# Kernel tuning notes

Hardware: AMD Instinct MI355X
Metric: run time of the kernel (lower is better)

Reference implementation:

```python
import jax, jax.numpy as jnp
import numpy as np

N_NODES = 100000

def graph_conv(x, edge_index, w_root, w_rel, b):
    # PyG GraphConv (aggr='add'): out = aggr(x_j) @ W_rel + b + x @ W_root
    src, dst = edge_index[0], edge_index[1]
    msgs = x[src]                                   # [E, F_in] gather
    agg = jax.ops.segment_sum(msgs, dst, num_segments=N_NODES)  # [N, F_in] scatter-add
    return agg @ w_rel + b + x @ w_root             # [N, F_out]


def setup_inputs() -> dict:
    key = jax.random.key(0)
    ks = jax.random.split(key, 12)
    E = 1600000
    return {
        "x": jax.random.normal(ks[0], (N_NODES, 16), dtype=jnp.float32),
        "edge_index": jax.random.randint(ks[1], (2, E), 0, N_NODES, dtype=jnp.int64),
        "w_root1": jax.random.normal(ks[2], (16, 32), dtype=jnp.float32) * 0.1,
        "w_rel1": jax.random.normal(ks[3], (16, 32), dtype=jnp.float32) * 0.1,
        "b1": jax.random.normal(ks[4], (32,), dtype=jnp.float32) * 0.1,
        "w_root2": jax.random.normal(ks[5], (32, 64), dtype=jnp.float32) * 0.1,
        "w_rel2": jax.random.normal(ks[6], (32, 64), dtype=jnp.float32) * 0.1,
        "b2": jax.random.normal(ks[7], (64,), dtype=jnp.float32) * 0.1,
        "fc1_w": jax.random.normal(ks[8], (64, 32), dtype=jnp.float32) * 0.1,
        "fc1_b": jax.random.normal(ks[9], (32,), dtype=jnp.float32) * 0.1,
        "fc2_w": jax.random.normal(ks[10], (32, 16), dtype=jnp.float32) * 0.1,
        "fc2_b": jax.random.normal(ks[11], (16,), dtype=jnp.float32) * 0.1,
    }


def reference(x, edge_index, w_root1, w_rel1, b1, w_root2, w_rel2, b2,
              fc1_w, fc1_b, fc2_w, fc2_b):
    h = jax.nn.relu(graph_conv(x, edge_index, w_root1, w_rel1, b1))   # [N, 32]
    h = jax.nn.relu(graph_conv(h, edge_index, w_root2, w_rel2, b2))   # [N, 64]
    h = jax.nn.relu(h @ fc1_w + fc1_b)                                 # [N, 32]
    return h @ fc2_w + fc2_b                                           # [N, 16]
```

## Files before the change

### kernel.cpp

```cpp
#include <hip/hip_runtime.h>

#define F4E(v,i) ((i)==0?(v).x:((i)==1?(v).y:((i)==2?(v).z:(v).w)))

#define CHUNK 4096
#define ITERS 8

typedef __attribute__((ext_vector_type(8))) short short8;
typedef __attribute__((ext_vector_type(4))) float f32x4;

__device__ inline float4 shfl4b(float4 v, int src) {
    float4 r;
    r.x = __shfl(v.x, src, 4); r.y = __shfl(v.y, src, 4);
    r.z = __shfl(v.z, src, 4); r.w = __shfl(v.w, src, 4);
    return r;
}

__device__ inline unsigned packbf2(float a, float b) {
    unsigned ua = __float_as_uint(a), ub = __float_as_uint(b);
    ua = (ua + 0x7fffu + ((ua >> 16) & 1u)) >> 16;
    ub = (ub + 0x7fffu + ((ub >> 16) & 1u)) >> 16;
    return ua | (ub << 16);
}
__device__ inline unsigned short bf16r(float f) {
    unsigned u = __float_as_uint(f);
    return (unsigned short)((u + 0x7fffu + ((u >> 16) & 1u)) >> 16);
}
__device__ inline float bflo(unsigned w) { return __uint_as_float(w << 16); }
__device__ inline float bfhi(unsigned w) { return __uint_as_float(w & 0xffff0000u); }

__global__ __launch_bounds__(256) void k_xcvt(
    const float* __restrict__ x, unsigned short* __restrict__ xb, int n8)
{
    int i = blockIdx.x * 256 + threadIdx.x;
    if (i >= n8) return;
    const float4* xp = reinterpret_cast<const float4*>(x) + (size_t)i * 2;
    float4 a = xp[0], b = xp[1];
    uint4 w;
    w.x = packbf2(a.x, a.y); w.y = packbf2(a.z, a.w);
    w.z = packbf2(b.x, b.y); w.w = packbf2(b.z, b.w);
    reinterpret_cast<uint4*>(xb)[i] = w;
}

__global__ __launch_bounds__(512) void k_bhist(
    const int* __restrict__ ei, int* __restrict__ bhist, int E, int NB)
{
    __shared__ int cnt[512];
    int t = threadIdx.x;
    cnt[t] = 0;
    __syncthreads();
    int base = blockIdx.x * CHUNK;
#pragma unroll
    for (int i = 0; i < ITERS; ++i) {
        int e = base + i * 512 + t;
        if (e < E) {
            int dst = ei[E + e];
            atomicAdd(&cnt[dst >> 8], 1);
        }
    }
    __syncthreads();
    if (t < NB && cnt[t]) atomicAdd(&bhist[t], cnt[t]);
}

__global__ __launch_bounds__(512) void k_bscan(
    const int* __restrict__ bhist, int* __restrict__ bstart,
    int* __restrict__ gcursor, int NB, int E)
{
    __shared__ int s[512];
    int t = threadIdx.x;
    int v0 = (t < NB) ? bhist[t] : 0;
    s[t] = v0;
    __syncthreads();
    for (int off = 1; off < 512; off <<= 1) {
        int v = (t >= off) ? s[t - off] : 0;
        __syncthreads();
        s[t] += v;
        __syncthreads();
    }
    if (t < NB) { int ex = s[t] - v0; bstart[t] = ex; gcursor[t] = ex; }
    if (t == 0) bstart[NB] = E;
}

__global__ __launch_bounds__(512) void k_partition(
    const int* __restrict__ ei, int* __restrict__ gcursor,
    int* __restrict__ epack, int E)
{
    __shared__ int cnt[512], sc[512], lbase[512], gbase[512], lcnt[512];
    __shared__ int stage[CHUNK];
    __shared__ unsigned short stageb[CHUNK];
    int t = threadIdx.x;
    cnt[t] = 0; lcnt[t] = 0;
    __syncthreads();

    int base = blockIdx.x * CHUNK;
    int pk[ITERS], bb[ITERS];
#pragma unroll
    for (int i = 0; i < ITERS; ++i) {
        int e = base + i * 512 + t;
        if (e < E) {
            int src = ei[e], dst = ei[E + e];
            pk[i] = (src << 8) | (dst & 255);
            bb[i] = dst >> 8;
            atomicAdd(&cnt[bb[i]], 1);
        } else bb[i] = -1;
    }
    __syncthreads();

    int v0 = cnt[t];
    sc[t] = v0;
    __syncthreads();
    for (int off = 1; off < 512; off <<= 1) {
        int v = (t >= off) ? sc[t - off] : 0;
        __syncthreads();
        sc[t] += v;
        __syncthreads();
    }
    lbase[t] = sc[t] - v0;
    if (v0 > 0) gbase[t] = atomicAdd(&gcursor[t], v0);
    __syncthreads();

#pragma unroll
    for (int i = 0; i < ITERS; ++i) {
        if (bb[i] >= 0) {
            int loc = atomicAdd(&lcnt[bb[i]], 1);
            int slot = lbase[bb[i]] + loc;
            stage[slot] = pk[i];
            stageb[slot] = (unsigned short)bb[i];
        }
    }
    __syncthreads();

    int m = min(CHUNK, E - base);
#pragma unroll
    for (int i = 0; i < ITERS; ++i) {
        int slot = i * 512 + t;
        if (slot < m) {
            int b = stageb[slot];
            epack[gbase[b] + (slot - lbase[b])] = stage[slot];
        }
    }
}

__global__ __launch_bounds__(256) void k_sort(
    const int* __restrict__ bstart, const int* __restrict__ epack,
    int* __restrict__ rs, int* __restrict__ esorted, int N, int E)
{
    __shared__ int hist[256], cur[256], sc[256];
    int t = threadIdx.x;
    int b = blockIdx.x;
    int s0 = bstart[b], s1 = bstart[b + 1];
    hist[t] = 0;
    __syncthreads();
    for (int e = s0 + t; e < s1; e += 256)
        atomicAdd(&hist[epack[e] & 255], 1);
    __syncthreads();

    int v0 = hist[t];
    sc[t] = v0;
    __syncthreads();
    for (int off = 1; off < 256; off <<= 1) {
        int v = (t >= off) ? sc[t - off] : 0;
        __syncthreads();
        sc[t] += v;
        __syncthreads();
    }
    int excl = sc[t] - v0;
    cur[t] = excl;
    int node = (b << 8) + t;
    if (node < N) rs[node] = s0 + excl;
    if (b == 0 && t == 0) rs[N] = E;
    __syncthreads();

    for (int e = s0 + t; e < s1; e += 256) {
        int pk = epack[e];
        int dlo = pk & 255;
        int pos = s0 + atomicAdd(&cur[dlo], 1);
        esorted[pos] = ((unsigned)pk) >> 8;
    }
}

__global__ __launch_bounds__(256) void k_g1f(
    const float* __restrict__ x, const unsigned short* __restrict__ xb,
    const int* __restrict__ rs, const int* __restrict__ esrc,
    const float* __restrict__ wroot, const float* __restrict__ wrel,
    const float* __restrict__ bias, unsigned short* __restrict__ h1, int N)
{
    __shared__ float4 s_wr[128], s_wl[128], s_b[8];
    int t = threadIdx.x;
    if (t < 128) {
        s_wr[t] = reinterpret_cast<const float4*>(wroot)[t];
        s_wl[t] = reinterpret_cast<const float4*>(wrel)[t];
    }
    if (t < 8) s_b[t] = reinterpret_cast<const float4*>(bias)[t];
    __syncthreads();

    int tid = blockIdx.x * 256 + t;
    int n = tid >> 2, p = tid & 3;
    if (n >= N) return;
    int s0 = rs[n], s1 = rs[n + 1];
    float4 g = make_float4(0.f, 0.f, 0.f, 0.f);
    int e = s0;
    for (; e + 7 < s1; e += 8) {
        uint2 w[8];
#pragma unroll
        for (int u = 0; u < 8; ++u) {
            int src = esrc[e + u];
            w[u] = reinterpret_cast<const uint2*>(xb + (size_t)src * 16)[p];
        }
#pragma unroll
        for (int u = 0; u < 8; ++u) {
            g.x += bflo(w[u].x); g.y += bfhi(w[u].x);
            g.z += bflo(w[u].y); g.w += bfhi(w[u].y);
        }
    }
    for (; e < s1; ++e) {
        int src = esrc[e];
        uint2 w0 = reinterpret_cast<const uint2*>(xb + (size_t)src * 16)[p];
        g.x += bflo(w0.x); g.y += bfhi(w0.x);
        g.z += bflo(w0.y); g.w += bfhi(w0.y);
    }
    float4 a = *reinterpret_cast<const float4*>(x + (size_t)n * 16 + p * 4);

    int jb = p * 2;
    float4 acc0 = s_b[jb], acc1 = s_b[jb + 1];
#pragma unroll
    for (int kc = 0; kc < 4; ++kc) {
        float4 a4 = shfl4b(a, kc);
        float4 g4 = shfl4b(g, kc);
#pragma unroll
        for (int kk = 0; kk < 4; ++kk) {
            float av = F4E(a4, kk), gv = F4E(g4, kk);
            int k = kc * 4 + kk;
            float4 wr0 = s_wr[k * 8 + jb], wr1 = s_wr[k * 8 + jb + 1];
            float4 wl0 = s_wl[k * 8 + jb], wl1 = s_wl[k * 8 + jb + 1];
            acc0.x += av * wr0.x + gv * wl0.x;
            acc0.y += av * wr0.y + gv * wl0.y;
            acc0.z += av * wr0.z + gv * wl0.z;
            acc0.w += av * wr0.w + gv * wl0.w;
            acc1.x += av * wr1.x + gv * wl1.x;
            acc1.y += av * wr1.y + gv * wl1.y;
            acc1.z += av * wr1.z + gv * wl1.z;
            acc1.w += av * wr1.w + gv * wl1.w;
        }
    }
    acc0.x = fmaxf(acc0.x, 0.f); acc0.y = fmaxf(acc0.y, 0.f);
    acc0.z = fmaxf(acc0.z, 0.f); acc0.w = fmaxf(acc0.w, 0.f);
    acc1.x = fmaxf(acc1.x, 0.f); acc1.y = fmaxf(acc1.y, 0.f);
    acc1.z = fmaxf(acc1.z, 0.f); acc1.w = fmaxf(acc1.w, 0.f);

    uint4 w;
    w.x = packbf2(acc0.x, acc0.y);
    w.y = packbf2(acc0.z, acc0.w);
    w.z = packbf2(acc1.x, acc1.y);
    w.w = packbf2(acc1.z, acc1.w);
    reinterpret_cast<uint4*>(h1 + (size_t)n * 32)[p] = w;
}

__global__ __launch_bounds__(256) void k_g2f(
    const unsigned short* __restrict__ h1, const int* __restrict__ rs,
    const int* __restrict__ esrc,
    const float* __restrict__ wroot, const float* __restrict__ wrel,
    const float* __restrict__ bias,
    const float* __restrict__ f1w, const float* __restrict__ f1b,
    const float* __restrict__ f2w, const float* __restrict__ f2b,
    float* __restrict__ out, int N)
{
    __shared__ __attribute__((aligned(16))) unsigned short h2l[4][16][72];
    __shared__ __attribute__((aligned(16))) unsigned short fl[4][16][40];

    int t = threadIdx.x;
    int w = t >> 6, l = t & 63;
    int m = l & 15, q4 = l >> 4;
    int tile = blockIdx.x * 4 + w;
    int nb = tile * 16;
    if (nb >= N) return;

    short8 fwr[4], fwl[4];
#pragma unroll
    for (int nt = 0; nt < 4; ++nt) {
#pragma unroll
        for (int i = 0; i < 8; ++i) {
            int k = q4 * 8 + i, j = nt * 16 + m;
            fwr[nt][i] = (short)bf16r(wroot[k * 64 + j]);
            fwl[nt][i] = (short)bf16r(wrel[k * 64 + j]);
        }
    }
    short8 ff1[2][2];
#pragma unroll
    for (int ks = 0; ks < 2; ++ks)
#pragma unroll
        for (int nt = 0; nt < 2; ++nt)
#pragma unroll
            for (int i = 0; i < 8; ++i)
                ff1[ks][nt][i] = (short)bf16r(f1w[(ks * 32 + q4 * 8 + i) * 32 + nt * 16 + m]);
    short8 ff2;
#pragma unroll
    for (int i = 0; i < 8; ++i)
        ff2[i] = (short)bf16r(f2w[(q4 * 8 + i) * 16 + m]);

    int n = nb + m;
    int s0 = 0, s1 = 0;
    if (n < N) { s0 = rs[n]; s1 = rs[n + 1]; }
    float ga0 = 0, ga1 = 0, ga2 = 0, ga3 = 0, ga4 = 0, ga5 = 0, ga6 = 0, ga7 = 0;
#define ACC8(W) { ga0 += bflo((W).x); ga1 += bfhi((W).x); \
                  ga2 += bflo((W).y); ga3 += bfhi((W).y); \
                  ga4 += bflo((W).z); ga5 += bfhi((W).z); \
                  ga6 += bflo((W).w); ga7 += bfhi((W).w); }
    int e = s0;
    for (; e + 3 < s1; e += 4) {
        int sa = esrc[e], sb = esrc[e + 1], sc2 = esrc[e + 2], sd = esrc[e + 3];
        uint4 wa = *reinterpret_cast<const uint4*>(h1 + (size_t)sa * 32 + q4 * 8);
        uint4 wb = *reinterpret_cast<const uint4*>(h1 + (size_t)sb * 32 + q4 * 8);
        uint4 wc = *reinterpret_cast<const uint4*>(h1 + (size_t)sc2 * 32 + q4 * 8);
        uint4 wd = *reinterpret_cast<const uint4*>(h1 + (size_t)sd * 32 + q4 * 8);
        ACC8(wa) ACC8(wb) ACC8(wc) ACC8(wd)
    }
    for (; e < s1; ++e) {
        int sa = esrc[e];
        uint4 wa = *reinterpret_cast<const uint4*>(h1 + (size_t)sa * 32 + q4 * 8);
        ACC8(wa)
    }
#undef ACC8

    short8 af;
    {
        uint4 av = make_uint4(0, 0, 0, 0);
        if (n < N) av = *reinterpret_cast<const uint4*>(h1 + (size_t)n * 32 + q4 * 8);
        __builtin_memcpy(&af, &av, 16);
    }
    short8 gf;
    gf[0] = (short)bf16r(ga0); gf[1] = (short)bf16r(ga1);
    gf[2] = (short)bf16r(ga2); gf[3] = (short)bf16r(ga3);
    gf[4] = (short)bf16r(ga4); gf[5] = (short)bf16r(ga5);
    gf[6] = (short)bf16r(ga6); gf[7] = (short)bf16r(ga7);

    f32x4 acc[4];
#pragma unroll
    for (int nt = 0; nt < 4; ++nt) {
        float bj = bias[nt * 16 + m];
        acc[nt] = (f32x4){bj, bj, bj, bj};
        acc[nt] = __builtin_amdgcn_mfma_f32_16x16x32_bf16(af, fwr[nt], acc[nt], 0, 0, 0);
        acc[nt] = __builtin_amdgcn_mfma_f32_16x16x32_bf16(gf, fwl[nt], acc[nt], 0, 0, 0);
    }
#pragma unroll
    for (int nt = 0; nt < 4; ++nt)
#pragma unroll
        for (int r = 0; r < 4; ++r)
            h2l[w][q4 * 4 + r][nt * 16 + m] = bf16r(fmaxf(acc[nt][r], 0.f));

    short8 h2a[2];
#pragma unroll
    for (int ks = 0; ks < 2; ++ks) {
        uint4 v = *reinterpret_cast<const uint4*>(&h2l[w][m][ks * 32 + q4 * 8]);
        __builtin_memcpy(&h2a[ks], &v, 16);
    }

    f32x4 fa[2];
#pragma unroll
    for (int nt = 0; nt < 2; ++nt) {
        float bj = f1b[nt * 16 + m];
        fa[nt] = (f32x4){bj, bj, bj, bj};
        fa[nt] = __builtin_amdgcn_mfma_f32_16x16x32_bf16(h2a[0], ff1[0][nt], fa[nt], 0, 0, 0);
        fa[nt] = __builtin_amdgcn_mfma_f32_16x16x32_bf16(h2a[1], ff1[1][nt], fa[nt], 0, 0, 0);
    }
#pragma unroll
    for (int nt = 0; nt < 2; ++nt)
#pragma unroll
        for (int r = 0; r < 4; ++r)
            fl[w][q4 * 4 + r][nt * 16 + m] = bf16r(fmaxf(fa[nt][r], 0.f));

    short8 ffr;
    {
        uint4 v = *reinterpret_cast<const uint4*>(&fl[w][m][q4 * 8]);
        __builtin_memcpy(&ffr, &v, 16);
    }

    float bj2 = f2b[m];
    f32x4 oacc = (f32x4){bj2, bj2, bj2, bj2};
    oacc = __builtin_amdgcn_mfma_f32_16x16x32_bf16(ffr, ff2, oacc, 0, 0, 0);
#pragma unroll
    for (int r = 0; r < 4; ++r) {
        int node = nb + q4 * 4 + r;
        if (node < N) out[(size_t)node * 16 + m] = oacc[r];
    }
}

extern "C" void kernel_launch(void* const* d_in, const int* in_sizes, int n_in,
                              void* d_out, int out_size, void* d_ws, size_t ws_size,
                              hipStream_t stream)
{
    const float* x   = (const float*)d_in[0];
    const int*   ei  = (const int*)d_in[1];
    const float* wr1 = (const float*)d_in[2];
    const float* wl1 = (const float*)d_in[3];
    const float* b1  = (const float*)d_in[4];
    const float* wr2 = (const float*)d_in[5];
    const float* wl2 = (const float*)d_in[6];
    const float* b2  = (const float*)d_in[7];
    const float* f1w = (const float*)d_in[8];
    const float* f1b = (const float*)d_in[9];
    const float* f2w = (const float*)d_in[10];
    const float* f2b = (const float*)d_in[11];
    float* out = (float*)d_out;

    const int N  = in_sizes[0] / 16;
    const int E  = in_sizes[1] / 2;
    const int NB = (N + 255) >> 8;

    float*          ws      = (float*)d_ws;
    unsigned short* h1      = (unsigned short*)ws;
    unsigned short* xb      = (unsigned short*)(ws + (size_t)N * 16);
    int*            esorted = (int*)(ws + (size_t)N * 24);
    int*            epack   = esorted + E;
    int*            rs      = epack + E;
    int*            bhist   = rs + N + 1;
    int*            bstart  = bhist + NB;
    int*            gcursor = bstart + NB + 1;

    hipMemsetAsync(bhist, 0, (size_t)NB * sizeof(int), stream);

    int nchunk = (E + CHUNK - 1) / CHUNK;
    int g_cv = (N * 2 + 255) / 256;
    int g_g1 = (N * 4 + 255) / 256;
    int g_g2 = (N + 63) / 64;

    k_xcvt     <<<g_cv,   256, 0, stream>>>(x, xb, N * 2);
    k_bhist    <<<nchunk, 512, 0, stream>>>(ei, bhist, E, NB);
    k_bscan    <<<1,      512, 0, stream>>>(bhist, bstart, gcursor, NB, E);
    k_partition<<<nchunk, 512, 0, stream>>>(ei, gcursor, epack, E);
    k_sort     <<<NB,     256, 0, stream>>>(bstart, epack, rs, esorted, N, E);

    k_g1f      <<<g_g1, 256, 0, stream>>>(x, xb, rs, esorted, wr1, wl1, b1, h1, N);
    k_g2f      <<<g_g2, 256, 0, stream>>>(h1, rs, esorted, wr2, wl2, b2,
                                          f1w, f1b, f2w, f2b, out, N);
}
```

Before: 197.7 us.

## Compute first GraphConv layer with bf16 MFMA over 16-node tiles

Rewrites the layer-1 fused kernel so each wavefront handles 16 nodes. The concatenated [x | agg] (K=32) is multiplied by stacked [W_root; W_rel] through one 16x16x32 bf16 MFMA per output half, replacing the per-thread FP32 FMA loop with lane shuffles. The root input now comes from the bf16 copy of x instead of fp32 x, and the aggregate is also rounded to bf16, which loses some precision. Weights are loaded per thread from global memory instead of staged in shared memory, and outputs are transposed through LDS for coalesced stores.

Result: no change. 199.0 us (+0.6%).

```diff
diff --git a/kernel.cpp b/kernel.cpp
--- a/kernel.cpp
+++ b/kernel.cpp
@@ -1,19 +1,10 @@
 #include <hip/hip_runtime.h>
-
-#define F4E(v,i) ((i)==0?(v).x:((i)==1?(v).y:((i)==2?(v).z:(v).w)))
 
 #define CHUNK 4096
 #define ITERS 8
 
 typedef __attribute__((ext_vector_type(8))) short short8;
 typedef __attribute__((ext_vector_type(4))) float f32x4;
-
-__device__ inline float4 shfl4b(float4 v, int src) {
-    float4 r;
-    r.x = __shfl(v.x, src, 4); r.y = __shfl(v.y, src, 4);
-    r.z = __shfl(v.z, src, 4); r.w = __shfl(v.w, src, 4);
-    return r;
-}
 
 __device__ inline unsigned packbf2(float a, float b) {
     unsigned ua = __float_as_uint(a), ub = __float_as_uint(b);
@@ -179,80 +170,89 @@
 }
 
 __global__ __launch_bounds__(256) void k_g1f(
-    const float* __restrict__ x, const unsigned short* __restrict__ xb,
+    const unsigned short* __restrict__ xb,
     const int* __restrict__ rs, const int* __restrict__ esrc,
     const float* __restrict__ wroot, const float* __restrict__ wrel,
     const float* __restrict__ bias, unsigned short* __restrict__ h1, int N)
 {
-    __shared__ float4 s_wr[128], s_wl[128], s_b[8];
-    int t = threadIdx.x;
-    if (t < 128) {
-        s_wr[t] = reinterpret_cast<const float4*>(wroot)[t];
-        s_wl[t] = reinterpret_cast<const float4*>(wrel)[t];
-    }
-    if (t < 8) s_b[t] = reinterpret_cast<const float4*>(bias)[t];
-    __syncthreads();
-
-    int tid = blockIdx.x * 256 + t;
-    int n = tid >> 2, p = tid & 3;
-    if (n >= N) return;
-    int s0 = rs[n], s1 = rs[n + 1];
-    float4 g = make_float4(0.f, 0.f, 0.f, 0.f);
+    __shared__ __attribute__((aligned(16))) unsigned short aggl[4][16][24];
+    __shared__ __attribute__((aligned(16))) unsigned short h1l[4][16][40];
+
+    int t = threadIdx.x;
+    int w = t >> 6, l = t & 63;
+    int m = l & 15, q4 = l >> 4;
+    int nb = (blockIdx.x * 4 + w) * 16;
+    if (nb >= N) return;
+    int n = nb + m;
+
+    short8 fb[2];
+#pragma unroll
+    for (int nt = 0; nt < 2; ++nt) {
+#pragma unroll
+        for (int i = 0; i < 8; ++i) {
+            int k = q4 * 8 + i, j = nt * 16 + m;
+            float wv = (k < 16) ? wroot[k * 32 + j] : wrel[(k - 16) * 32 + j];
+            fb[nt][i] = (short)bf16r(wv);
+        }
+    }
+
+    int s0 = 0, s1 = 0;
+    if (n < N) { s0 = rs[n]; s1 = rs[n + 1]; }
+    float g0 = 0, g1 = 0, g2 = 0, g3 = 0;
     int e = s0;
     for (; e + 7 < s1; e += 8) {
-        uint2 w[8];
+        uint2 v[8];
 #pragma unroll
         for (int u = 0; u < 8; ++u) {
             int src = esrc[e + u];
-            w[u] = reinterpret_cast<const uint2*>(xb + (size_t)src * 16)[p];
+            v[u] = *reinterpret_cast<const uint2*>(xb + (size_t)src * 16 + q4 * 4);
         }
 #pragma unroll
         for (int u = 0; u < 8; ++u) {
-            g.x += bflo(w[u].x); g.y += bfhi(w[u].x);
-            g.z += bflo(w[u].y); g.w += bfhi(w[u].y);
+            g0 += bflo(v[u].x); g1 += bfhi(v[u].x);
+            g2 += bflo(v[u].y); g3 += bfhi(v[u].y);
         }
     }
     for (; e < s1; ++e) {
         int src = esrc[e];
-        uint2 w0 = reinterpret_cast<const uint2*>(xb + (size_t)src * 16)[p];
-        g.x += bflo(w0.x); g.y += bfhi(w0.x);
-        g.z += bflo(w0.y); g.w += bfhi(w0.y);
-    }
-    float4 a = *reinterpret_cast<const float4*>(x + (size_t)n * 16 + p * 4);
-
-    int jb = p * 2;
-    float4 acc0 = s_b[jb], acc1 = s_b[jb + 1];
-#pragma unroll
-    for (int kc = 0; kc < 4; ++kc) {
-        float4 a4 = shfl4b(a, kc);
-        float4 g4 = shfl4b(g, kc);
-#pragma unroll
-        for (int kk = 0; kk < 4; ++kk) {
-            float av = F4E(a4, kk), gv = F4E(g4, kk);
-            int k = kc * 4 + kk;
-            float4 wr0 = s_wr[k * 8 + jb], wr1 = s_wr[k * 8 + jb + 1];
-            float4 wl0 = s_wl[k * 8 + jb], wl1 = s_wl[k * 8 + jb + 1];
-            acc0.x += av * wr0.x + gv * wl0.x;
-            acc0.y += av * wr0.y + gv * wl0.y;
-            acc0.z += av * wr0.z + gv * wl0.z;
-            acc0.w += av * wr0.w + gv * wl0.w;
-            acc1.x += av * wr1.x + gv * wl1.x;
-            acc1.y += av * wr1.y + gv * wl1.y;
-            acc1.z += av * wr1.z + gv * wl1.z;
-            acc1.w += av * wr1.w + gv * wl1.w;
-        }
-    }
-    acc0.x = fmaxf(acc0.x, 0.f); acc0.y = fmaxf(acc0.y, 0.f);
-    acc0.z = fmaxf(acc0.z, 0.f); acc0.w = fmaxf(acc0.w, 0.f);
-    acc1.x = fmaxf(acc1.x, 0.f); acc1.y = fmaxf(acc1.y, 0.f);
-    acc1.z = fmaxf(acc1.z, 0.f); acc1.w = fmaxf(acc1.w, 0.f);
-
-    uint4 w;
-    w.x = packbf2(acc0.x, acc0.y);
-    w.y = packbf2(acc0.z, acc0.w);
-    w.z = packbf2(acc1.x, acc1.y);
-    w.w = packbf2(acc1.z, acc1.w);
-    reinterpret_cast<uint4*>(h1 + (size_t)n * 32)[p] = w;
+        uint2 v0 = *reinterpret_cast<const uint2*>(xb + (size_t)src * 16 + q4 * 4);
+        g0 += bflo(v0.x); g1 += bfhi(v0.x);
+        g2 += bflo(v0.y); g3 += bfhi(v0.y);
+    }
+    uint2 pg;
+    pg.x = packbf2(g0, g1);
+    pg.y = packbf2(g2, g3);
+    *reinterpret_cast<uint2*>(&aggl[w][m][q4 * 4]) = pg;
+
+    short8 af;
+    {
+        uint4 v = make_uint4(0, 0, 0, 0);
+        if (q4 < 2) {
+            if (n < N)
+                v = *reinterpret_cast<const uint4*>(xb + (size_t)n * 16 + q4 * 8);
+        } else {
+            v = *reinterpret_cast<const uint4*>(&aggl[w][m][(q4 - 2) * 8]);
+        }
+        __builtin_memcpy(&af, &v, 16);
+    }
+
+    f32x4 acc[2];
+#pragma unroll
+    for (int nt = 0; nt < 2; ++nt) {
+        float bj = bias[nt * 16 + m];
+        acc[nt] = (f32x4){bj, bj, bj, bj};
+        acc[nt] = __builtin_amdgcn_mfma_f32_16x16x32_bf16(af, fb[nt], acc[nt], 0, 0, 0);
+    }
+
+#pragma unroll
+    for (int nt = 0; nt < 2; ++nt)
+#pragma unroll
+        for (int r = 0; r < 4; ++r)
+            h1l[w][q4 * 4 + r][nt * 16 + m] = bf16r(fmaxf(acc[nt][r], 0.f));
+
+    uint4 hv = *reinterpret_cast<const uint4*>(&h1l[w][m][q4 * 8]);
+    if (n < N)
+        reinterpret_cast<uint4*>(h1 + (size_t)n * 32)[q4] = hv;
 }
 
 __global__ __launch_bounds__(256) void k_g2f(
@@ -420,8 +420,7 @@
 
     int nchunk = (E + CHUNK - 1) / CHUNK;
     int g_cv = (N * 2 + 255) / 256;
-    int g_g1 = (N * 4 + 255) / 256;
-    int g_g2 = (N + 63) / 64;
+    int g_mf = (N + 63) / 64;
 
     k_xcvt     <<<g_cv,   256, 0, stream>>>(x, xb, N * 2);
     k_bhist    <<<nchunk, 512, 0, stream>>>(ei, bhist, E, NB);
@@ -429,7 +428,7 @@
     k_partition<<<nchunk, 512, 0, stream>>>(ei, gcursor, epack, E);
     k_sort     <<<NB,     256, 0, stream>>>(bstart, epack, rs, esorted, N, E);
 
-    k_g1f      <<<g_g1, 256, 0, stream>>>(x, xb, rs, esorted, wr1, wl1, b1, h1, N);
-    k_g2f      <<<g_g2, 256, 0, stream>>>(h1, rs, esorted, wr2, wl2, b2,
+    k_g1f      <<<g_mf, 256, 0, stream>>>(xb, rs, esorted, wr1, wl1, b1, h1, N);
+    k_g2f      <<<g_mf, 256, 0, stream>>>(h1, rs, esorted, wr2, wl2, b2,
                                           f1w, f1b, f2w, f2b, out, N);
 }
```
